# Performance work log

Hardware: AMD Instinct MI355X
Metric: run time of the kernel (lower is better)

## Reference

```python
import jax, jax.numpy as jnp
import numpy as np

N, IN_F, OUT_F, K = 256, 8192, 8320, 16
J = OUT_F - IN_F  # 128


def setup_inputs() -> dict:
    key = jax.random.key(0)
    k1, k2 = jax.random.split(key)
    tensor = jax.random.normal(k1, (N, IN_F), dtype=jnp.float32)
    T = jax.random.normal(k2, (IN_F, J, K), dtype=jnp.float32)
    return {"tensor": tensor, "T": T}


def reference(tensor, T):
    # flatten(start_dim=1) is identity for rank-2 input
    x = tensor.reshape(tensor.shape[0], -1)            # [N, IN_F]
    feats = jnp.einsum('ni,ijk->njk', x, T)            # [N, J, K]
    # pairwise L1 across batch: [N,1,J,K] - [N,J,K] -> [N,N,J,K]
    diff = jnp.abs(feats[:, None, :, :] - feats[None, :, :, :])
    l1 = jnp.sum(diff, axis=3)                         # [N, N, J]
    diversity = jnp.sum(jnp.exp(-l1), axis=1)          # [N, J]
    return jnp.concatenate((x, diversity), axis=1)     # [N, IN_F + J]
```

## Files before the change

### kernel.cpp

```cpp
#include <hip/hip_runtime.h>

typedef unsigned int  u32;
typedef unsigned short u16;

typedef __bf16 bf16x8 __attribute__((ext_vector_type(8)));
typedef float  floatx4 __attribute__((ext_vector_type(4)));

#define N_ROWS 256
#define IN_F   8192
#define OUT_F  8320
#define JDIM   128
#define KDIM   16
#define JK     2048

#define BM     256
#define BN     64
#define BK     64
#define WSTRIDE 72

#define SLAB_U16   (N_ROWS * JK)
#define JSLICE_U16 (N_ROWS * KDIM)

typedef const __attribute__((address_space(1))) u32 gu32;
typedef __attribute__((address_space(3))) u32 su32;

__device__ __forceinline__ u16 f2bf(float f) {
    u32 u = __float_as_uint(f);
    return (u16)((u + 0x7fffu + ((u >> 16) & 1u)) >> 16);
}
__device__ __forceinline__ float bf2f(u16 h) { return __uint_as_float(((u32)h) << 16); }

__global__ __launch_bounds__(256) void prep_kernel(const float* __restrict__ X,
                                                   float* __restrict__ out,
                                                   u16* __restrict__ Xb)
{
    int t = blockIdx.x * 256 + threadIdx.x;
    float4 v = reinterpret_cast<const float4*>(X)[t];
    int row = t >> 11;
    int c4  = t & 2047;
    reinterpret_cast<float4*>(out + (size_t)row * OUT_F)[c4] = v;
    ushort4 b;
    b.x = f2bf(v.x); b.y = f2bf(v.y); b.z = f2bf(v.z); b.w = f2bf(v.w);
    reinterpret_cast<ushort4*>(Xb)[t] = b;
    if (t < 8192) {
        int r2 = t >> 5, j4 = t & 31;
        reinterpret_cast<float4*>(out + (size_t)r2 * OUT_F + IN_F)[j4] = make_float4(0.f, 0.f, 0.f, 0.f);
    }
}

__global__ __launch_bounds__(256) void gemm_kernel(const u16* __restrict__ Xb,
                                                   const float* __restrict__ W,
                                                   u16* __restrict__ slabs,
                                                   int kchunk)
{
    __shared__ u16 xs[BM * BK];
    __shared__ u16 wt[BN * WSTRIDE];

    const int tid  = threadIdx.x;
    const int lane = tid & 63;
    const int wave = tid >> 6;
    const int c0   = blockIdx.x * BN;
    const int s    = blockIdx.y;
    const int k0base = s * kchunk;

    floatx4 acc[4][4] = {};

    const int xrl = lane >> 3;
    const int xgc = (lane & 7) ^ xrl;
    const int wk  = (tid >> 4) << 2;
    const int wc  = (tid & 15) << 2;

    const float* wptr = W + (size_t)(k0base + wk) * JK + c0 + wc;

    float4 wreg[4];
    #pragma unroll
    for (int r = 0; r < 4; ++r)
        wreg[r] = *(const float4*)(wptr + (size_t)r * JK);

    const int iters = kchunk >> 6;
    for (int it = 0; it < iters; ++it) {
        const int k0 = k0base + it * BK;
        __syncthreads();

        #pragma unroll
        for (int g = 0; g < 8; ++g) {
            int rbase = wave * 64 + g * 8;
            const u16* gp = Xb + (size_t)(rbase + xrl) * IN_F + k0 + xgc * 8;
            u32* lp = (u32*)&xs[rbase * BK];
            __builtin_amdgcn_global_load_lds((gu32*)gp, (su32*)lp, 16, 0, 0);
        }

        {
            const float* wr = (const float*)wreg;
            #pragma unroll
            for (int i = 0; i < 4; ++i) {
                u32 lo = (u32)f2bf(wr[0 * 4 + i]) | ((u32)f2bf(wr[1 * 4 + i]) << 16);
                u32 hi = (u32)f2bf(wr[2 * 4 + i]) | ((u32)f2bf(wr[3 * 4 + i]) << 16);
                uint2 v; v.x = lo; v.y = hi;
                *(uint2*)&wt[(wc + i) * WSTRIDE + wk] = v;
            }
        }
        __syncthreads();

        if (it + 1 < iters) {
            const float* wn = wptr + (size_t)(it + 1) * BK * JK;
            #pragma unroll
            for (int r = 0; r < 4; ++r)
                wreg[r] = *(const float4*)(wn + (size_t)r * JK);
        }

        const int mrow = lane & 15;
        const int q    = lane >> 4;
        #pragma unroll
        for (int h = 0; h < 2; ++h) {
            bf16x8 a[4], b[4];
            #pragma unroll
            for (int rt = 0; rt < 4; ++rt) {
                int rl   = wave * 64 + rt * 16 + mrow;
                int slot = (h * 4 + q) ^ (rl & 7);
                a[rt] = *reinterpret_cast<const bf16x8*>(&xs[rl * BK + slot * 8]);
            }
            #pragma unroll
            for (int ct = 0; ct < 4; ++ct) {
                int col = ct * 16 + mrow;
                b[ct] = *reinterpret_cast<const bf16x8*>(&wt[col * WSTRIDE + (h * 4 + q) * 8]);
            }
            #pragma unroll
            for (int rt = 0; rt < 4; ++rt)
                #pragma unroll
                for (int ct = 0; ct < 4; ++ct)
                    acc[rt][ct] = __builtin_amdgcn_mfma_f32_16x16x32_bf16(a[rt], b[ct], acc[rt][ct], 0, 0, 0);
        }
    }

    const int qe = lane >> 4;
    const int cl = lane & 15;
    u16* sp = slabs + (size_t)s * SLAB_U16;
    #pragma unroll
    for (int rt = 0; rt < 4; ++rt)
        #pragma unroll
        for (int ct = 0; ct < 4; ++ct) {
            int j = (c0 >> 4) + ct;
            #pragma unroll
            for (int r = 0; r < 4; ++r) {
                int row = wave * 64 + rt * 16 + qe * 4 + r;
                sp[(size_t)j * JSLICE_U16 + row * KDIM + cl] = f2bf(acc[rt][ct][r]);
            }
        }
}

template<int S>
__global__ __launch_bounds__(256) void fused_rp_kernel(const u16* __restrict__ slabs,
                                                       float* __restrict__ out)
{
    const int j  = blockIdx.x;
    const int mq = blockIdx.y;
    const int n  = threadIdx.x;

    __shared__ float F[N_ROWS * KDIM];

    const u16* base = slabs + (size_t)j * JSLICE_U16 + n * KDIM;

    float f[16];
    #pragma unroll
    for (int k = 0; k < 16; ++k) f[k] = 0.f;

    #pragma unroll
    for (int so = 0; so < S; so += 4) {
        uint4 va[4], vb[4];
        #pragma unroll
        for (int i = 0; i < 4; ++i) {
            const u16* p = base + (size_t)(so + i) * SLAB_U16;
            va[i] = *(const uint4*)p;
            vb[i] = *(const uint4*)(p + 8);
        }
        #pragma unroll
        for (int i = 0; i < 4; ++i) {
            const u16* ha = (const u16*)&va[i];
            const u16* hb = (const u16*)&vb[i];
            #pragma unroll
            for (int e = 0; e < 8; ++e) {
                f[e]     += bf2f(ha[e]);
                f[8 + e] += bf2f(hb[e]);
            }
        }
    }

    float4* Fp = (float4*)&F[n * KDIM];
    Fp[0] = make_float4(f[0],  f[1],  f[2],  f[3]);
    Fp[1] = make_float4(f[4],  f[5],  f[6],  f[7]);
    Fp[2] = make_float4(f[8],  f[9],  f[10], f[11]);
    Fp[3] = make_float4(f[12], f[13], f[14], f[15]);
    __syncthreads();

    float accum = 0.f;
    const int m0 = mq * 64;
    #pragma unroll 2
    for (int m = 0; m < 64; ++m) {
        const float* Fm = &F[(m0 + m) * KDIM];
        float l1 = 0.f;
        #pragma unroll
        for (int k = 0; k < 16; ++k) l1 += fabsf(f[k] - Fm[k]);
        accum += exp2f(-1.4426950408889634f * l1);
    }
    atomicAdd(&out[(size_t)n * OUT_F + IN_F + j], accum);
}

extern "C" void kernel_launch(void* const* d_in, const int* in_sizes, int n_in,
                              void* d_out, int out_size, void* d_ws, size_t ws_size,
                              hipStream_t stream)
{
    const float* X = (const float*)d_in[0];
    const float* T = (const float*)d_in[1];
    float* out = (float*)d_out;

    u16* Xb    = (u16*)d_ws;
    u16* slabs = (u16*)((char*)d_ws + (4u << 20));

    int S = 16;
    if (ws_size < (4u << 20) + (size_t)16 * SLAB_U16 * 2) S = 8;
    if (ws_size < (4u << 20) + (size_t)8  * SLAB_U16 * 2) S = 4;
    int kchunk = IN_F / S;

    prep_kernel<<<2048, 256, 0, stream>>>(X, out, Xb);
    gemm_kernel<<<dim3(JK / BN, S), 256, 0, stream>>>(Xb, T, slabs, kchunk);
    if (S == 16)
        fused_rp_kernel<16><<<dim3(JDIM, 4), 256, 0, stream>>>(slabs, out);
    else if (S == 8)
        fused_rp_kernel<8><<<dim3(JDIM, 4), 256, 0, stream>>>(slabs, out);
    else
        fused_rp_kernel<4><<<dim3(JDIM, 4), 256, 0, stream>>>(slabs, out);
}
```

Measured before the change: 135.5 us.

## Fold prep kernel into GEMM and reduction kernels, converting X in-register

Removes the separate prep kernel. The GEMM now loads fp32 X directly, converts it to bf16 with packed cvt instructions, and writes it to padded LDS instead of reading a pre-converted bf16 copy through global_load_lds. The zeroing of the diversity columns moves into the GEMM's s==0 blocks, and the copy of X into the output moves into the pairwise kernel. This saves a launch and the bf16 workspace round trip, but every K-split block now reads twice as many bytes of X from fp32 and re-converts it, and register pressure rises under launch_bounds(256,2).

```diff
diff --git a/kernel.cpp b/kernel.cpp
--- a/kernel.cpp
+++ b/kernel.cpp
@@ -16,13 +16,11 @@
 #define BM     256
 #define BN     64
 #define BK     64
+#define XSTRIDE 72
 #define WSTRIDE 72
 
 #define SLAB_U16   (N_ROWS * JK)
 #define JSLICE_U16 (N_ROWS * KDIM)
-
-typedef const __attribute__((address_space(1))) u32 gu32;
-typedef __attribute__((address_space(3))) u32 su32;
 
 __device__ __forceinline__ u16 f2bf(float f) {
     u32 u = __float_as_uint(f);
@@ -30,79 +28,94 @@
 }
 __device__ __forceinline__ float bf2f(u16 h) { return __uint_as_float(((u32)h) << 16); }
 
-__global__ __launch_bounds__(256) void prep_kernel(const float* __restrict__ X,
-                                                   float* __restrict__ out,
-                                                   u16* __restrict__ Xb)
+__device__ __forceinline__ u32 cvtpk(float lo, float hi) {
+    u32 d;
+    asm("v_cvt_pk_bf16_f32 %0, %1, %2" : "=v"(d) : "v"(lo), "v"(hi));
+    return d;
+}
+
+template<int S>
+__global__ __launch_bounds__(256, 2) void gemm_kernel(const float* __restrict__ X,
+                                                      const float* __restrict__ W,
+                                                      u16* __restrict__ slabs,
+                                                      float* __restrict__ out)
 {
-    int t = blockIdx.x * 256 + threadIdx.x;
-    float4 v = reinterpret_cast<const float4*>(X)[t];
-    int row = t >> 11;
-    int c4  = t & 2047;
-    reinterpret_cast<float4*>(out + (size_t)row * OUT_F)[c4] = v;
-    ushort4 b;
-    b.x = f2bf(v.x); b.y = f2bf(v.y); b.z = f2bf(v.z); b.w = f2bf(v.w);
-    reinterpret_cast<ushort4*>(Xb)[t] = b;
-    if (t < 8192) {
-        int r2 = t >> 5, j4 = t & 31;
-        reinterpret_cast<float4*>(out + (size_t)r2 * OUT_F + IN_F)[j4] = make_float4(0.f, 0.f, 0.f, 0.f);
-    }
-}
-
-__global__ __launch_bounds__(256) void gemm_kernel(const u16* __restrict__ Xb,
-                                                   const float* __restrict__ W,
-                                                   u16* __restrict__ slabs,
-                                                   int kchunk)
-{
-    __shared__ u16 xs[BM * BK];
-    __shared__ u16 wt[BN * WSTRIDE];
+    constexpr int KCH   = IN_F / S;
+    constexpr int ITERS = KCH >> 6;
+
+    __shared__ __align__(16) u16 xs[BM * XSTRIDE];
+    __shared__ __align__(16) u16 wt[BN * WSTRIDE];
 
     const int tid  = threadIdx.x;
     const int lane = tid & 63;
     const int wave = tid >> 6;
     const int c0   = blockIdx.x * BN;
     const int s    = blockIdx.y;
-    const int k0base = s * kchunk;
+    const int k0base = s * KCH;
+
+    if (s == 0) {
+        int g = blockIdx.x * 256 + tid;
+        int r2 = g >> 5, j4 = g & 31;
+        reinterpret_cast<float4*>(out + (size_t)r2 * OUT_F + IN_F)[j4] =
+            make_float4(0.f, 0.f, 0.f, 0.f);
+    }
 
     floatx4 acc[4][4] = {};
 
-    const int xrl = lane >> 3;
-    const int xgc = (lane & 7) ^ xrl;
-    const int wk  = (tid >> 4) << 2;
-    const int wc  = (tid & 15) << 2;
-
+    const int xr = lane >> 3;
+    const int xc = lane & 7;
+    const float* xptr = X + (size_t)(wave * 64 + xr) * IN_F + k0base + xc * 8;
+
+    const int wk = (tid >> 4) << 2;
+    const int wc = (tid & 15) << 2;
     const float* wptr = W + (size_t)(k0base + wk) * JK + c0 + wc;
 
+    float4 xreg[16];
     float4 wreg[4];
+    #pragma unroll
+    for (int i = 0; i < 8; ++i) {
+        const float* p = xptr + (size_t)i * 8 * IN_F;
+        xreg[2 * i]     = ((const float4*)p)[0];
+        xreg[2 * i + 1] = ((const float4*)p)[1];
+    }
     #pragma unroll
     for (int r = 0; r < 4; ++r)
         wreg[r] = *(const float4*)(wptr + (size_t)r * JK);
 
-    const int iters = kchunk >> 6;
-    for (int it = 0; it < iters; ++it) {
-        const int k0 = k0base + it * BK;
+    for (int it = 0; it < ITERS; ++it) {
         __syncthreads();
 
         #pragma unroll
-        for (int g = 0; g < 8; ++g) {
-            int rbase = wave * 64 + g * 8;
-            const u16* gp = Xb + (size_t)(rbase + xrl) * IN_F + k0 + xgc * 8;
-            u32* lp = (u32*)&xs[rbase * BK];
-            __builtin_amdgcn_global_load_lds((gu32*)gp, (su32*)lp, 16, 0, 0);
+        for (int i = 0; i < 8; ++i) {
+            int row = wave * 64 + i * 8 + xr;
+            uint4 q;
+            q.x = cvtpk(xreg[2 * i].x,     xreg[2 * i].y);
+            q.y = cvtpk(xreg[2 * i].z,     xreg[2 * i].w);
+            q.z = cvtpk(xreg[2 * i + 1].x, xreg[2 * i + 1].y);
+            q.w = cvtpk(xreg[2 * i + 1].z, xreg[2 * i + 1].w);
+            *(uint4*)&xs[row * XSTRIDE + xc * 8] = q;
         }
 
         {
             const float* wr = (const float*)wreg;
             #pragma unroll
             for (int i = 0; i < 4; ++i) {
-                u32 lo = (u32)f2bf(wr[0 * 4 + i]) | ((u32)f2bf(wr[1 * 4 + i]) << 16);
-                u32 hi = (u32)f2bf(wr[2 * 4 + i]) | ((u32)f2bf(wr[3 * 4 + i]) << 16);
-                uint2 v; v.x = lo; v.y = hi;
+                uint2 v;
+                v.x = cvtpk(wr[0 * 4 + i], wr[1 * 4 + i]);
+                v.y = cvtpk(wr[2 * 4 + i], wr[3 * 4 + i]);
                 *(uint2*)&wt[(wc + i) * WSTRIDE + wk] = v;
             }
         }
         __syncthreads();
 
-        if (it + 1 < iters) {
+        if (it + 1 < ITERS) {
+            const float* xn = xptr + (size_t)(it + 1) * BK;
+            #pragma unroll
+            for (int i = 0; i < 8; ++i) {
+                const float* p = xn + (size_t)i * 8 * IN_F;
+                xreg[2 * i]     = ((const float4*)p)[0];
+                xreg[2 * i + 1] = ((const float4*)p)[1];
+            }
             const float* wn = wptr + (size_t)(it + 1) * BK * JK;
             #pragma unroll
             for (int r = 0; r < 4; ++r)
@@ -116,9 +129,8 @@
             bf16x8 a[4], b[4];
             #pragma unroll
             for (int rt = 0; rt < 4; ++rt) {
-                int rl   = wave * 64 + rt * 16 + mrow;
-                int slot = (h * 4 + q) ^ (rl & 7);
-                a[rt] = *reinterpret_cast<const bf16x8*>(&xs[rl * BK + slot * 8]);
+                int rl = wave * 64 + rt * 16 + mrow;
+                a[rt] = *reinterpret_cast<const bf16x8*>(&xs[rl * XSTRIDE + (h * 4 + q) * 8]);
             }
             #pragma unroll
             for (int ct = 0; ct < 4; ++ct) {
@@ -151,11 +163,14 @@
 
 template<int S>
 __global__ __launch_bounds__(256) void fused_rp_kernel(const u16* __restrict__ slabs,
+                                                       const float* __restrict__ X,
                                                        float* __restrict__ out)
 {
     const int j  = blockIdx.x;
     const int mq = blockIdx.y;
     const int n  = threadIdx.x;
+    const int lin = blockIdx.y * JDIM + blockIdx.x;
+    const int g0  = lin * 256 + n;
 
     __shared__ float F[N_ROWS * KDIM];
 
@@ -169,13 +184,13 @@
     for (int so = 0; so < S; so += 4) {
         uint4 va[4], vb[4];
         #pragma unroll
-        for (int i = 0; i < 4; ++i) {
+        for (int i = 0; i < 4 && so + i < S; ++i) {
             const u16* p = base + (size_t)(so + i) * SLAB_U16;
             va[i] = *(const uint4*)p;
             vb[i] = *(const uint4*)(p + 8);
         }
         #pragma unroll
-        for (int i = 0; i < 4; ++i) {
+        for (int i = 0; i < 4 && so + i < S; ++i) {
             const u16* ha = (const u16*)&va[i];
             const u16* hb = (const u16*)&vb[i];
             #pragma unroll
@@ -191,6 +206,12 @@
     Fp[1] = make_float4(f[4],  f[5],  f[6],  f[7]);
     Fp[2] = make_float4(f[8],  f[9],  f[10], f[11]);
     Fp[3] = make_float4(f[12], f[13], f[14], f[15]);
+
+    float4 cp[4];
+    #pragma unroll
+    for (int i = 0; i < 4; ++i)
+        cp[i] = reinterpret_cast<const float4*>(X)[g0 + i * 131072];
+
     __syncthreads();
 
     float accum = 0.f;
@@ -204,6 +225,13 @@
         accum += exp2f(-1.4426950408889634f * l1);
     }
     atomicAdd(&out[(size_t)n * OUT_F + IN_F + j], accum);
+
+    #pragma unroll
+    for (int i = 0; i < 4; ++i) {
+        int t = g0 + i * 131072;
+        int row = t >> 11, c4 = t & 2047;
+        reinterpret_cast<float4*>(out + (size_t)row * OUT_F)[c4] = cp[i];
+    }
 }
 
 extern "C" void kernel_launch(void* const* d_in, const int* in_sizes, int n_in,
@@ -214,20 +242,20 @@
     const float* T = (const float*)d_in[1];
     float* out = (float*)d_out;
 
-    u16* Xb    = (u16*)d_ws;
-    u16* slabs = (u16*)((char*)d_ws + (4u << 20));
+    u16* slabs = (u16*)d_ws;
 
     int S = 16;
-    if (ws_size < (4u << 20) + (size_t)16 * SLAB_U16 * 2) S = 8;
-    if (ws_size < (4u << 20) + (size_t)8  * SLAB_U16 * 2) S = 4;
-    int kchunk = IN_F / S;
-
-    prep_kernel<<<2048, 256, 0, stream>>>(X, out, Xb);
-    gemm_kernel<<<dim3(JK / BN, S), 256, 0, stream>>>(Xb, T, slabs, kchunk);
-    if (S == 16)
-        fused_rp_kernel<16><<<dim3(JDIM, 4), 256, 0, stream>>>(slabs, out);
-    else if (S == 8)
-        fused_rp_kernel<8><<<dim3(JDIM, 4), 256, 0, stream>>>(slabs, out);
-    else
-        fused_rp_kernel<4><<<dim3(JDIM, 4), 256, 0, stream>>>(slabs, out);
-}
+    if (ws_size < (size_t)16 * SLAB_U16 * 2) S = 8;
+    if (ws_size < (size_t)8  * SLAB_U16 * 2) S = 4;
+
+    if (S == 16) {
+        gemm_kernel<16><<<dim3(JK / BN, 16), 256, 0, stream>>>(X, T, slabs, out);
+        fused_rp_kernel<16><<<dim3(JDIM, 4), 256, 0, stream>>>(slabs, X, out);
+    } else if (S == 8) {
+        gemm_kernel<8><<<dim3(JK / BN, 8), 256, 0, stream>>>(X, T, slabs, out);
+        fused_rp_kernel<8><<<dim3(JDIM, 4), 256, 0, stream>>>(slabs, X, out);
+    } else {
+        gemm_kernel<4><<<dim3(JK / BN, 4), 256, 0, stream>>>(X, T, slabs, out);
+        fused_rp_kernel<4><<<dim3(JDIM, 4), 256, 0, stream>>>(slabs, X, out);
+    }
+}
```

Measured after the change: 154.6 us. +14.1%, slower.
